# Performance work log

Measured on AMD Instinct MI355X. Metric: run time of the kernel, lower is better.

## Reference

```python
import jax, jax.numpy as jnp
import numpy as np

K_HOPS = 2  # SGConv K = nlayers


def setup_inputs() -> dict:
    key = jax.random.key(0)
    k1, k2, k3 = jax.random.split(key, 3)
    N, E, F, C = 100000, 1600000, 128, 40
    x = jax.random.normal(k1, (N, F), dtype=jnp.float32)
    edge_index = jax.random.randint(k2, (2, E), 0, N, dtype=jnp.int64)
    W = jax.random.normal(k3, (C, F), dtype=jnp.float32) * (1.0 / np.sqrt(F))
    b = jnp.zeros((C,), dtype=jnp.float32)
    return {"x": x, "edge_index": edge_index, "W": W, "b": b}


def reference(x, edge_index, W, b):
    # SGConv: K hops of GCN-normalized propagation (with self-loops), then Linear.
    N = x.shape[0]
    loop = jnp.arange(N, dtype=edge_index.dtype)
    src = jnp.concatenate([edge_index[0], loop])  # message source
    dst = jnp.concatenate([edge_index[1], loop])  # aggregation target
    w = jnp.ones(src.shape[0], dtype=x.dtype)     # edge_weight=None -> 1, self-loop fill=1
    deg = jax.ops.segment_sum(w, dst, num_segments=N)  # in-degree incl. self-loop (>=1)
    dinv = jax.lax.rsqrt(deg)
    norm = dinv[src] * w * dinv[dst]              # D^{-1/2} A D^{-1/2}
    h = x
    for _ in range(K_HOPS):
        h = jax.ops.segment_sum(norm[:, None] * h[src], dst, num_segments=N)
    return h @ W.T + b
```

## Files before the change

### kernel.cpp

```cpp
#include <hip/hip_runtime.h>
#include <hip/hip_fp16.h>
#include <cstdint>

#define CDIM 40
#define FDIM 128
#define BIN_SHIFT 8
#define BIN_SZ (1 << BIN_SHIFT)
#define CHUNK 4096
#define STAGE_CAP 8192

typedef _Float16 f16x8 __attribute__((ext_vector_type(8)));
typedef float f32x4 __attribute__((ext_vector_type(4)));

static __device__ __forceinline__ long long load_idx(const void* p, int is64, long long i) {
    if (is64) return ((const long long*)p)[i];
    return (long long)((const int*)p)[i];
}

static __device__ __forceinline__ unsigned packh2(float a, float b) {
    __half2 h;
    h.x = __float2half(a);
    h.y = __float2half(b);
    return *(unsigned*)&h;
}

static __device__ __forceinline__ void addv2(float* acc, uint2 v) {
    const __half2* h = (const __half2*)&v;
    float2 f0 = __half22float2(h[0]);
    float2 f1 = __half22float2(h[1]);
    acc[0] += f0.x; acc[1] += f0.y; acc[2] += f1.x; acc[3] += f1.y;
}

static __device__ __forceinline__ f16x8 cvt8(float4 a, float4 b) {
    f16x8 r;
    r[0] = (_Float16)a.x; r[1] = (_Float16)a.y; r[2] = (_Float16)a.z; r[3] = (_Float16)a.w;
    r[4] = (_Float16)b.x; r[5] = (_Float16)b.y; r[6] = (_Float16)b.z; r[7] = (_Float16)b.w;
    return r;
}

__global__ void k_init(int* cursor, int nb, int capRec) {
    int i = blockIdx.x * blockDim.x + threadIdx.x;
    if (i < nb) cursor[i] = i * capRec;
}

__global__ __launch_bounds__(256) void kA3(const void* ei, long long E,
                                           int nb, int* __restrict__ cursor,
                                           unsigned* __restrict__ binned) {
    __shared__ unsigned lval[CHUNK];
    __shared__ unsigned short lbin[CHUNK];
    __shared__ int lcnt[512];
    __shared__ int lbase[512];
    __shared__ int lflag;
    int tid = threadIdx.x;
    if (tid == 0) lflag = 1;
    for (int i = tid; i < nb; i += 256) lcnt[i] = 0;
    __syncthreads();
    {
        const unsigned* w = (const unsigned*)ei;
        int nscan = (int)((2 * E < 4096) ? (2 * E) : 4096);
        for (int k = 1 + 2 * tid; k < nscan; k += 512)
            if (w[k] != 0u) lflag = 0;
    }
    __syncthreads();
    int is64 = lflag;
    long long base = (long long)blockIdx.x * CHUNK;
    int nk = (int)min((long long)CHUNK, E - base);
    for (int k = tid; k < nk; k += 256) {
        long long e = base + k;
        int s = (int)load_idx(ei, is64, e);
        int d = (int)load_idx(ei, is64, E + e);
        int bin = d >> BIN_SHIFT;
        lval[k] = (unsigned)s | ((unsigned)(d & (BIN_SZ - 1)) << 17);
        lbin[k] = (unsigned short)bin;
        atomicAdd(&lcnt[bin], 1);
    }
    __syncthreads();
    for (int i = tid; i < nb; i += 256) {
        int c = lcnt[i];
        lbase[i] = c ? atomicAdd(&cursor[i], c) : 0;
        lcnt[i] = 0;
    }
    __syncthreads();
    for (int k = tid; k < nk; k += 256) {
        int bin = lbin[k];
        int loc = atomicAdd(&lcnt[bin], 1);
        binned[lbase[bin] + loc] = lval[k];
    }
}

__global__ __launch_bounds__(256) void kB(const unsigned* __restrict__ binned,
                                          const int* __restrict__ cursor,
                                          int capRec, int capC,
                                          int2* __restrict__ meta,
                                          float* __restrict__ dinv,
                                          int* __restrict__ cursorG,
                                          int* __restrict__ csr, int N) {
    __shared__ int lcnt[BIN_SZ];
    __shared__ int lexcl[BIN_SZ];
    __shared__ int ls[256];
    __shared__ int dh[64];
    __shared__ int tot;
    __shared__ int stage[STAGE_CAP];
    int b = blockIdx.x, tid = threadIdx.x;
    int node0 = b << BIN_SHIFT;
    int nn = min(BIN_SZ, N - node0);
    int recBase = b * capRec;
    int csrBase = b * capC;
    int nedges = cursor[b] - recBase;

    lcnt[tid] = 0;
    if (tid < 64) dh[tid] = 0;
    __syncthreads();
    for (int t = tid; t < nedges; t += 256)
        atomicAdd(&lcnt[(binned[recBase + t] >> 17) & (BIN_SZ - 1)], 1);
    __syncthreads();
    int myc = lcnt[tid];
    int psz = (myc + 3) & ~3;
    ls[tid] = psz;
    __syncthreads();
    for (int off = 1; off < 256; off <<= 1) {
        int t = (tid >= off) ? ls[tid - off] : 0;
        __syncthreads();
        ls[tid] += t;
        __syncthreads();
    }
    int ex = ls[tid] - psz;
    lexcl[tid] = ex;
    if (tid == 255) tot = ls[255];
    if (tid < nn) {
        dinv[node0 + tid] = rsqrtf(1.0f + (float)myc);
        atomicAdd(&dh[min(myc, 63)], 1);
    }
    __syncthreads();
    int total = tot;
    int dv = (tid < 64) ? dh[tid] : 0;
    ls[tid] = dv;
    __syncthreads();
    for (int off = 1; off < 64; off <<= 1) {
        int t = (tid >= off) ? ls[tid - off] : 0;
        __syncthreads();
        ls[tid] += t;
        __syncthreads();
    }
    if (tid < 64) dh[tid] = ls[tid] - dv;
    __syncthreads();
    if (tid < nn) {
        int pos = atomicAdd(&dh[min(myc, 63)], 1);
        int2 mi;
        mi.x = csrBase + ex;
        mi.y = (node0 + tid) | (myc << 17);
        meta[node0 + pos] = mi;
    }
    __syncthreads();
    lcnt[tid] = ex;
    __syncthreads();
    if (total <= STAGE_CAP) {
        for (int t = tid; t < total; t += 256) stage[t] = N;
        __syncthreads();
        for (int t = tid; t < nedges; t += 256) {
            unsigned v = binned[recBase + t];
            int src = (int)(v & 0x1FFFFu);
            int dl  = (int)((v >> 17) & (BIN_SZ - 1));
            int p = atomicAdd(&lcnt[dl], 1);
            stage[p] = src;
        }
        __syncthreads();
        const int4* sp = (const int4*)stage;
        int4* cp = (int4*)(csr + csrBase);
        for (int t = tid; t < (total >> 2); t += 256) cp[t] = sp[t];
    } else {
        if (tid < nn) cursorG[node0 + tid] = csrBase + ex;
        __syncthreads();
        for (int t = tid; t < nedges; t += 256) {
            unsigned v = binned[recBase + t];
            int src = (int)(v & 0x1FFFFu);
            int dl  = (int)((v >> 17) & (BIN_SZ - 1));
            int p = atomicAdd(&cursorG[node0 + dl], 1);
            csr[p] = src;
        }
        if (tid < nn)
            for (int k = myc; k < psz; ++k) csr[csrBase + ex + k] = N;
    }
}

__global__ __launch_bounds__(256) void k_gemm(const float* __restrict__ x,
                                              const float* __restrict__ W,
                                              const float* __restrict__ dinv,
                                              __half* __restrict__ gA,
                                              __half* __restrict__ gB, int N) {
    if (blockIdx.x == 0 && threadIdx.x < 20) {
        if (threadIdx.x < 16) ((unsigned*)(gA + (size_t)N * 32))[threadIdx.x] = 0u;
        else                  ((unsigned*)(gB + (size_t)N * 8))[threadIdx.x - 16] = 0u;
    }
    int wave = threadIdx.x >> 6;
    int lane = threadIdx.x & 63;
    int m = lane & 15;
    int quad = lane >> 4;
    f16x8 bfrag[3][4];
#pragma unroll
    for (int t = 0; t < 3; ++t) {
        int c = t * 16 + m;
#pragma unroll
        for (int q = 0; q < 4; ++q) {
            if (c < CDIM) {
                const float* wp = W + (size_t)c * FDIM + q * 32 + quad * 8;
                float4 w0 = *(const float4*)wp;
                float4 w1 = *(const float4*)(wp + 4);
                bfrag[t][q] = cvt8(w0, w1);
            } else {
                f16x8 z = {0, 0, 0, 0, 0, 0, 0, 0};
                bfrag[t][q] = z;
            }
        }
    }
#pragma unroll
    for (int i = 0; i < 4; ++i) {
        int nodebase = blockIdx.x * 256 + wave * 64 + i * 16;
        if (nodebase >= N) break;
        const float* xp = x + (size_t)(nodebase + m) * FDIM + quad * 8;
        f16x8 afrag[4];
#pragma unroll
        for (int q = 0; q < 4; ++q) {
            float4 x0 = *(const float4*)(xp + q * 32);
            float4 x1 = *(const float4*)(xp + q * 32 + 4);
            afrag[q] = cvt8(x0, x1);
        }
        f32x4 acc0 = {0, 0, 0, 0}, acc1 = {0, 0, 0, 0}, acc2 = {0, 0, 0, 0};
#pragma unroll
        for (int q = 0; q < 4; ++q) {
            acc0 = __builtin_amdgcn_mfma_f32_16x16x32_f16(afrag[q], bfrag[0][q], acc0, 0, 0, 0);
            acc1 = __builtin_amdgcn_mfma_f32_16x16x32_f16(afrag[q], bfrag[1][q], acc1, 0, 0, 0);
            acc2 = __builtin_amdgcn_mfma_f32_16x16x32_f16(afrag[q], bfrag[2][q], acc2, 0, 0, 0);
        }
        float4 dvv = *(const float4*)&dinv[nodebase + quad * 4];
        float ds[4] = {dvv.x, dvv.y, dvv.z, dvv.w};
#pragma unroll
        for (int r = 0; r < 4; ++r) {
            int node = nodebase + quad * 4 + r;
            gA[(size_t)node * 32 + m]      = __float2half(acc0[r] * ds[r]);
            gA[(size_t)node * 32 + 16 + m] = __float2half(acc1[r] * ds[r]);
            if (m < 8)
                gB[(size_t)node * 8 + m]   = __float2half(acc2[r] * ds[r]);
        }
    }
}

__global__ __launch_bounds__(256) void k_gather(const int2* __restrict__ meta,
                                                const int* __restrict__ csr,
                                                const __half* __restrict__ gA,
                                                const __half* __restrict__ gB,
                                                const float* __restrict__ b,
                                                __half* __restrict__ goA,
                                                __half* __restrict__ goB,
                                                float* __restrict__ outF,
                                                int N, int mode) {
    unsigned t = blockIdx.x * 256 + threadIdx.x;
    if (mode == 0 && t < 20) {
        if (t < 16) ((unsigned*)(goA + (size_t)N * 32))[t] = 0u;
        else        ((unsigned*)(goB + (size_t)N * 8))[t - 16] = 0u;
    }
    unsigned gidx = t / 10, c = t - gidx * 10;
    if (gidx >= (unsigned)N) return;
    int2 mi = meta[gidx];
    int j = mi.x;
    int node = mi.y & 0x1FFFF;
    int deg = mi.y >> 17;
    int end_pad = j + ((deg + 3) & ~3);
    const uint2* src;
    unsigned stride;
    if (c < 8) { src = (const uint2*)gA + c;       stride = 8; }
    else       { src = (const uint2*)gB + (c - 8); stride = 2; }
    float acc[4] = {0.0f, 0.0f, 0.0f, 0.0f};
    addv2(acc, src[(size_t)node * stride]);
    for (; j + 8 <= end_pad; j += 8) {
        int4 c0 = *(const int4*)&csr[j];
        int4 c1 = *(const int4*)&csr[j + 4];
        uint2 v0 = src[(size_t)c0.x * stride];
        uint2 v1 = src[(size_t)c0.y * stride];
        uint2 v2 = src[(size_t)c0.z * stride];
        uint2 v3 = src[(size_t)c0.w * stride];
        uint2 v4 = src[(size_t)c1.x * stride];
        uint2 v5 = src[(size_t)c1.y * stride];
        uint2 v6 = src[(size_t)c1.z * stride];
        uint2 v7 = src[(size_t)c1.w * stride];
        addv2(acc, v0); addv2(acc, v1); addv2(acc, v2); addv2(acc, v3);
        addv2(acc, v4); addv2(acc, v5); addv2(acc, v6); addv2(acc, v7);
    }
    if (j < end_pad) {
        int4 c0 = *(const int4*)&csr[j];
        uint2 v0 = src[(size_t)c0.x * stride];
        uint2 v1 = src[(size_t)c0.y * stride];
        uint2 v2 = src[(size_t)c0.z * stride];
        uint2 v3 = src[(size_t)c0.w * stride];
        addv2(acc, v0); addv2(acc, v1); addv2(acc, v2); addv2(acc, v3);
    }
    float d = rsqrtf(1.0f + (float)deg);
    if (mode == 0) {
        float s = d * d;
        uint2 o;
        o.x = packh2(acc[0] * s, acc[1] * s);
        o.y = packh2(acc[2] * s, acc[3] * s);
        if (c < 8) ((uint2*)goA)[(size_t)node * 8 + c] = o;
        else       ((uint2*)goB)[(size_t)node * 2 + (c - 8)] = o;
    } else {
        float4 bv = ((const float4*)b)[c];
        float4 o;
        o.x = acc[0] * d + bv.x;
        o.y = acc[1] * d + bv.y;
        o.z = acc[2] * d + bv.z;
        o.w = acc[3] * d + bv.w;
        ((float4*)outF)[(size_t)node * 10 + c] = o;
    }
}

static inline size_t align256(size_t v) { return (v + 255) & ~(size_t)255; }

extern "C" void kernel_launch(void* const* d_in, const int* in_sizes, int n_in,
                              void* d_out, int out_size, void* d_ws, size_t ws_size,
                              hipStream_t stream) {
    const float* x  = (const float*)d_in[0];
    const void*  ei = d_in[1];
    const float* W  = (const float*)d_in[2];
    const float* b  = (const float*)d_in[3];
    float* out = (float*)d_out;

    const int N = in_sizes[0] / FDIM;
    const long long E = (long long)in_sizes[1] / 2;

    const int nb     = (N + BIN_SZ - 1) >> BIN_SHIFT;
    const int nchunk = (int)((E + CHUNK - 1) / CHUNK);
    int capRec = (int)(E / nb) + 2048;
    if (capRec > STAGE_CAP) capRec = STAGE_CAP;
    int capC = (capRec + BIN_SZ * 3 + 1027) & ~3;

    char* wsb = (char*)d_ws;
    size_t off = 0;
    int*      cursor  = (int*)(wsb + off);      off = align256(off + (size_t)nb * 4);
    int*      cursorG = (int*)(wsb + off);      off = align256(off + (size_t)N * 4);
    int2*     meta    = (int2*)(wsb + off);     off = align256(off + (size_t)N * 8);
    float*    dinv    = (float*)(wsb + off);    off = align256(off + (size_t)N * 4);
    __half*   gA0     = (__half*)(wsb + off);   off = align256(off + (size_t)(N + 1) * 32 * 2);
    __half*   gB0     = (__half*)(wsb + off);   off = align256(off + (size_t)(N + 1) * 8 * 2);
    __half*   gA1     = (__half*)(wsb + off);   off = align256(off + (size_t)(N + 1) * 32 * 2);
    __half*   gB1     = (__half*)(wsb + off);   off = align256(off + (size_t)(N + 1) * 8 * 2);
    unsigned* binned  = (unsigned*)(wsb + off); off = align256(off + (size_t)nb * capRec * 4);
    int*      csr     = (int*)(wsb + off);      off = align256(off + (size_t)nb * capC * 4);

    const int B = 256;
    const int nbGE = (N + 255) / 256;
    const unsigned GT = 10u * (unsigned)N;
    const int nbGA = (int)((GT + B - 1) / B);

    k_init  <<<(nb + 255) / 256, 256, 0, stream>>>(cursor, nb, capRec);
    kA3     <<<nchunk, B, 0, stream>>>(ei, E, nb, cursor, binned);
    kB      <<<nb, B, 0, stream>>>(binned, cursor, capRec, capC, meta, dinv, cursorG, csr, N);
    k_gemm  <<<nbGE, B, 0, stream>>>(x, W, dinv, gA0, gB0, N);
    k_gather<<<nbGA, B, 0, stream>>>(meta, csr, gA0, gB0, b, gA1, gB1, nullptr, N, 0);
    k_gather<<<nbGA, B, 0, stream>>>(meta, csr, gA1, gB1, b, nullptr, nullptr, out, N, 1);
}
```

Measured before the change: 214.5 us.

## Split 40-channel propagated features into two 20-channel halves gathered separately

The projected fp16 features are now stored as two separate 20-channel arrays (40 bytes per node each) instead of a 32+8 split. Each hop runs two gather passes, one per half, so each pass's random-access working set is half the size and more likely to stay in L2/MALL. csr index loads and output stores become nontemporal to avoid polluting cache. The cost is reading the CSR index array twice per hop, doubled kernel launches, and 40-byte rows that are not aligned to 64-byte lines.

```diff
diff --git a/kernel.cpp b/kernel.cpp
--- a/kernel.cpp
+++ b/kernel.cpp
@@ -11,6 +11,8 @@
 
 typedef _Float16 f16x8 __attribute__((ext_vector_type(8)));
 typedef float f32x4 __attribute__((ext_vector_type(4)));
+typedef int i32x4 __attribute__((ext_vector_type(4)));
+typedef unsigned u32x2 __attribute__((ext_vector_type(2)));
 
 static __device__ __forceinline__ long long load_idx(const void* p, int is64, long long i) {
     if (is64) return ((const long long*)p)[i];
@@ -186,11 +188,11 @@
 __global__ __launch_bounds__(256) void k_gemm(const float* __restrict__ x,
                                               const float* __restrict__ W,
                                               const float* __restrict__ dinv,
-                                              __half* __restrict__ gA,
-                                              __half* __restrict__ gB, int N) {
+                                              __half* __restrict__ gL,
+                                              __half* __restrict__ gH, int N) {
     if (blockIdx.x == 0 && threadIdx.x < 20) {
-        if (threadIdx.x < 16) ((unsigned*)(gA + (size_t)N * 32))[threadIdx.x] = 0u;
-        else                  ((unsigned*)(gB + (size_t)N * 8))[threadIdx.x - 16] = 0u;
+        if (threadIdx.x < 10) ((unsigned*)(gL + (size_t)N * 20))[threadIdx.x] = 0u;
+        else                  ((unsigned*)(gH + (size_t)N * 20))[threadIdx.x - 10] = 0u;
     }
     int wave = threadIdx.x >> 6;
     int lane = threadIdx.x & 63;
@@ -237,79 +239,74 @@
 #pragma unroll
         for (int r = 0; r < 4; ++r) {
             int node = nodebase + quad * 4 + r;
-            gA[(size_t)node * 32 + m]      = __float2half(acc0[r] * ds[r]);
-            gA[(size_t)node * 32 + 16 + m] = __float2half(acc1[r] * ds[r]);
+            float v0 = acc0[r] * ds[r];
+            float v1 = acc1[r] * ds[r];
+            gL[(size_t)node * 20 + m] = __float2half(v0);
+            if (m < 4) gL[(size_t)node * 20 + 16 + m] = __float2half(v1);
+            else       gH[(size_t)node * 20 + (m - 4)] = __float2half(v1);
             if (m < 8)
-                gB[(size_t)node * 8 + m]   = __float2half(acc2[r] * ds[r]);
+                gH[(size_t)node * 20 + 12 + m] = __float2half(acc2[r] * ds[r]);
         }
     }
 }
 
 __global__ __launch_bounds__(256) void k_gather(const int2* __restrict__ meta,
                                                 const int* __restrict__ csr,
-                                                const __half* __restrict__ gA,
-                                                const __half* __restrict__ gB,
+                                                const __half* __restrict__ gin,
                                                 const float* __restrict__ b,
-                                                __half* __restrict__ goA,
-                                                __half* __restrict__ goB,
+                                                __half* __restrict__ gout,
                                                 float* __restrict__ outF,
-                                                int N, int mode) {
+                                                int N, int mode, int pass) {
     unsigned t = blockIdx.x * 256 + threadIdx.x;
-    if (mode == 0 && t < 20) {
-        if (t < 16) ((unsigned*)(goA + (size_t)N * 32))[t] = 0u;
-        else        ((unsigned*)(goB + (size_t)N * 8))[t - 16] = 0u;
-    }
-    unsigned gidx = t / 10, c = t - gidx * 10;
+    if (mode == 0 && t < 10)
+        ((unsigned*)(gout + (size_t)N * 20))[t] = 0u;
+    unsigned gidx = t / 5, c = t - gidx * 5;
     if (gidx >= (unsigned)N) return;
     int2 mi = meta[gidx];
     int j = mi.x;
     int node = mi.y & 0x1FFFF;
     int deg = mi.y >> 17;
     int end_pad = j + ((deg + 3) & ~3);
-    const uint2* src;
-    unsigned stride;
-    if (c < 8) { src = (const uint2*)gA + c;       stride = 8; }
-    else       { src = (const uint2*)gB + (c - 8); stride = 2; }
+    const uint2* src = (const uint2*)gin + c;
     float acc[4] = {0.0f, 0.0f, 0.0f, 0.0f};
-    addv2(acc, src[(size_t)node * stride]);
+    addv2(acc, src[(size_t)node * 5]);
     for (; j + 8 <= end_pad; j += 8) {
-        int4 c0 = *(const int4*)&csr[j];
-        int4 c1 = *(const int4*)&csr[j + 4];
-        uint2 v0 = src[(size_t)c0.x * stride];
-        uint2 v1 = src[(size_t)c0.y * stride];
-        uint2 v2 = src[(size_t)c0.z * stride];
-        uint2 v3 = src[(size_t)c0.w * stride];
-        uint2 v4 = src[(size_t)c1.x * stride];
-        uint2 v5 = src[(size_t)c1.y * stride];
-        uint2 v6 = src[(size_t)c1.z * stride];
-        uint2 v7 = src[(size_t)c1.w * stride];
+        i32x4 c0 = __builtin_nontemporal_load((const i32x4*)&csr[j]);
+        i32x4 c1 = __builtin_nontemporal_load((const i32x4*)&csr[j + 4]);
+        uint2 v0 = src[(size_t)c0.x * 5];
+        uint2 v1 = src[(size_t)c0.y * 5];
+        uint2 v2 = src[(size_t)c0.z * 5];
+        uint2 v3 = src[(size_t)c0.w * 5];
+        uint2 v4 = src[(size_t)c1.x * 5];
+        uint2 v5 = src[(size_t)c1.y * 5];
+        uint2 v6 = src[(size_t)c1.z * 5];
+        uint2 v7 = src[(size_t)c1.w * 5];
         addv2(acc, v0); addv2(acc, v1); addv2(acc, v2); addv2(acc, v3);
         addv2(acc, v4); addv2(acc, v5); addv2(acc, v6); addv2(acc, v7);
     }
     if (j < end_pad) {
-        int4 c0 = *(const int4*)&csr[j];
-        uint2 v0 = src[(size_t)c0.x * stride];
-        uint2 v1 = src[(size_t)c0.y * stride];
-        uint2 v2 = src[(size_t)c0.z * stride];
-        uint2 v3 = src[(size_t)c0.w * stride];
+        i32x4 c0 = __builtin_nontemporal_load((const i32x4*)&csr[j]);
+        uint2 v0 = src[(size_t)c0.x * 5];
+        uint2 v1 = src[(size_t)c0.y * 5];
+        uint2 v2 = src[(size_t)c0.z * 5];
+        uint2 v3 = src[(size_t)c0.w * 5];
         addv2(acc, v0); addv2(acc, v1); addv2(acc, v2); addv2(acc, v3);
     }
     float d = rsqrtf(1.0f + (float)deg);
     if (mode == 0) {
         float s = d * d;
-        uint2 o;
+        u32x2 o;
         o.x = packh2(acc[0] * s, acc[1] * s);
         o.y = packh2(acc[2] * s, acc[3] * s);
-        if (c < 8) ((uint2*)goA)[(size_t)node * 8 + c] = o;
-        else       ((uint2*)goB)[(size_t)node * 2 + (c - 8)] = o;
+        __builtin_nontemporal_store(o, (u32x2*)gout + (size_t)node * 5 + c);
     } else {
-        float4 bv = ((const float4*)b)[c];
-        float4 o;
-        o.x = acc[0] * d + bv.x;
-        o.y = acc[1] * d + bv.y;
-        o.z = acc[2] * d + bv.z;
-        o.w = acc[3] * d + bv.w;
-        ((float4*)outF)[(size_t)node * 10 + c] = o;
+        float4 bv = ((const float4*)(b + pass * 20))[c];
+        f32x4 o;
+        o[0] = acc[0] * d + bv.x;
+        o[1] = acc[1] * d + bv.y;
+        o[2] = acc[2] * d + bv.z;
+        o[3] = acc[3] * d + bv.w;
+        __builtin_nontemporal_store(o, (f32x4*)outF + (size_t)node * 10 + pass * 5 + c);
     }
 }
 
@@ -339,22 +336,24 @@
     int*      cursorG = (int*)(wsb + off);      off = align256(off + (size_t)N * 4);
     int2*     meta    = (int2*)(wsb + off);     off = align256(off + (size_t)N * 8);
     float*    dinv    = (float*)(wsb + off);    off = align256(off + (size_t)N * 4);
-    __half*   gA0     = (__half*)(wsb + off);   off = align256(off + (size_t)(N + 1) * 32 * 2);
-    __half*   gB0     = (__half*)(wsb + off);   off = align256(off + (size_t)(N + 1) * 8 * 2);
-    __half*   gA1     = (__half*)(wsb + off);   off = align256(off + (size_t)(N + 1) * 32 * 2);
-    __half*   gB1     = (__half*)(wsb + off);   off = align256(off + (size_t)(N + 1) * 8 * 2);
+    __half*   g0L     = (__half*)(wsb + off);   off = align256(off + (size_t)(N + 1) * 20 * 2);
+    __half*   g0H     = (__half*)(wsb + off);   off = align256(off + (size_t)(N + 1) * 20 * 2);
+    __half*   g1L     = (__half*)(wsb + off);   off = align256(off + (size_t)(N + 1) * 20 * 2);
+    __half*   g1H     = (__half*)(wsb + off);   off = align256(off + (size_t)(N + 1) * 20 * 2);
     unsigned* binned  = (unsigned*)(wsb + off); off = align256(off + (size_t)nb * capRec * 4);
     int*      csr     = (int*)(wsb + off);      off = align256(off + (size_t)nb * capC * 4);
 
     const int B = 256;
     const int nbGE = (N + 255) / 256;
-    const unsigned GT = 10u * (unsigned)N;
+    const unsigned GT = 5u * (unsigned)N;
     const int nbGA = (int)((GT + B - 1) / B);
 
     k_init  <<<(nb + 255) / 256, 256, 0, stream>>>(cursor, nb, capRec);
     kA3     <<<nchunk, B, 0, stream>>>(ei, E, nb, cursor, binned);
     kB      <<<nb, B, 0, stream>>>(binned, cursor, capRec, capC, meta, dinv, cursorG, csr, N);
-    k_gemm  <<<nbGE, B, 0, stream>>>(x, W, dinv, gA0, gB0, N);
-    k_gather<<<nbGA, B, 0, stream>>>(meta, csr, gA0, gB0, b, gA1, gB1, nullptr, N, 0);
-    k_gather<<<nbGA, B, 0, stream>>>(meta, csr, gA1, gB1, b, nullptr, nullptr, out, N, 1);
-}
+    k_gemm  <<<nbGE, B, 0, stream>>>(x, W, dinv, g0L, g0H, N);
+    k_gather<<<nbGA, B, 0, stream>>>(meta, csr, g0L, b, g1L, nullptr, N, 0, 0);
+    k_gather<<<nbGA, B, 0, stream>>>(meta, csr, g0H, b, g1H, nullptr, N, 0, 1);
+    k_gather<<<nbGA, B, 0, stream>>>(meta, csr, g1L, b, nullptr, out, N, 1, 0);
+    k_gather<<<nbGA, B, 0, stream>>>(meta, csr, g1H, b, nullptr, out, N, 1, 1);
+}
```

After: 252.9 us. 17.9% more time.

## Fuse all stages into one persistent cooperative kernel with grid syncs

Applied to the files above, without the earlier changes.

Replaces the six separate launches (init, binning, CSR build, GEMM, two gather hops) with a single persistent cooperative kernel that loops over work and separates phases with grid.sync. The GEMM is also folded into the CSR-build loop per bin, using a shared-memory dinv, so the dinv global round trip is dropped. The aim is to cut launch gaps and inter-kernel tails. In exchange, occupancy is limited by the larger shared-memory union, and grid-wide barriers plus fewer resident blocks may reduce latency hiding in the gather phases. The old multi-kernel path stays as a fallback.

```diff
diff --git a/kernel.cpp b/kernel.cpp
--- a/kernel.cpp
+++ b/kernel.cpp
@@ -1,4 +1,5 @@
 #include <hip/hip_runtime.h>
+#include <hip/hip_cooperative_groups.h>
 #include <hip/hip_fp16.h>
 #include <cstdint>
 
@@ -12,6 +13,8 @@
 typedef _Float16 f16x8 __attribute__((ext_vector_type(8)));
 typedef float f32x4 __attribute__((ext_vector_type(4)));
 
+namespace cg = cooperative_groups;
+
 static __device__ __forceinline__ long long load_idx(const void* p, int is64, long long i) {
     if (is64) return ((const long long*)p)[i];
     return (long long)((const int*)p)[i];
@@ -38,229 +41,51 @@
     return r;
 }
 
-__global__ void k_init(int* cursor, int nb, int capRec) {
-    int i = blockIdx.x * blockDim.x + threadIdx.x;
-    if (i < nb) cursor[i] = i * capRec;
-}
-
-__global__ __launch_bounds__(256) void kA3(const void* ei, long long E,
-                                           int nb, int* __restrict__ cursor,
-                                           unsigned* __restrict__ binned) {
-    __shared__ unsigned lval[CHUNK];
-    __shared__ unsigned short lbin[CHUNK];
-    __shared__ int lcnt[512];
-    __shared__ int lbase[512];
-    __shared__ int lflag;
-    int tid = threadIdx.x;
-    if (tid == 0) lflag = 1;
-    for (int i = tid; i < nb; i += 256) lcnt[i] = 0;
-    __syncthreads();
-    {
-        const unsigned* w = (const unsigned*)ei;
-        int nscan = (int)((2 * E < 4096) ? (2 * E) : 4096);
-        for (int k = 1 + 2 * tid; k < nscan; k += 512)
-            if (w[k] != 0u) lflag = 0;
-    }
-    __syncthreads();
-    int is64 = lflag;
-    long long base = (long long)blockIdx.x * CHUNK;
-    int nk = (int)min((long long)CHUNK, E - base);
-    for (int k = tid; k < nk; k += 256) {
-        long long e = base + k;
-        int s = (int)load_idx(ei, is64, e);
-        int d = (int)load_idx(ei, is64, E + e);
-        int bin = d >> BIN_SHIFT;
-        lval[k] = (unsigned)s | ((unsigned)(d & (BIN_SZ - 1)) << 17);
-        lbin[k] = (unsigned short)bin;
-        atomicAdd(&lcnt[bin], 1);
-    }
-    __syncthreads();
-    for (int i = tid; i < nb; i += 256) {
-        int c = lcnt[i];
-        lbase[i] = c ? atomicAdd(&cursor[i], c) : 0;
-        lcnt[i] = 0;
-    }
-    __syncthreads();
-    for (int k = tid; k < nk; k += 256) {
-        int bin = lbin[k];
-        int loc = atomicAdd(&lcnt[bin], 1);
-        binned[lbase[bin] + loc] = lval[k];
-    }
-}
-
-__global__ __launch_bounds__(256) void kB(const unsigned* __restrict__ binned,
-                                          const int* __restrict__ cursor,
-                                          int capRec, int capC,
-                                          int2* __restrict__ meta,
-                                          float* __restrict__ dinv,
-                                          int* __restrict__ cursorG,
-                                          int* __restrict__ csr, int N) {
-    __shared__ int lcnt[BIN_SZ];
-    __shared__ int lexcl[BIN_SZ];
-    __shared__ int ls[256];
-    __shared__ int dh[64];
-    __shared__ int tot;
-    __shared__ int stage[STAGE_CAP];
-    int b = blockIdx.x, tid = threadIdx.x;
-    int node0 = b << BIN_SHIFT;
-    int nn = min(BIN_SZ, N - node0);
-    int recBase = b * capRec;
-    int csrBase = b * capC;
-    int nedges = cursor[b] - recBase;
-
-    lcnt[tid] = 0;
-    if (tid < 64) dh[tid] = 0;
-    __syncthreads();
-    for (int t = tid; t < nedges; t += 256)
-        atomicAdd(&lcnt[(binned[recBase + t] >> 17) & (BIN_SZ - 1)], 1);
-    __syncthreads();
-    int myc = lcnt[tid];
-    int psz = (myc + 3) & ~3;
-    ls[tid] = psz;
-    __syncthreads();
-    for (int off = 1; off < 256; off <<= 1) {
-        int t = (tid >= off) ? ls[tid - off] : 0;
-        __syncthreads();
-        ls[tid] += t;
-        __syncthreads();
-    }
-    int ex = ls[tid] - psz;
-    lexcl[tid] = ex;
-    if (tid == 255) tot = ls[255];
-    if (tid < nn) {
-        dinv[node0 + tid] = rsqrtf(1.0f + (float)myc);
-        atomicAdd(&dh[min(myc, 63)], 1);
-    }
-    __syncthreads();
-    int total = tot;
-    int dv = (tid < 64) ? dh[tid] : 0;
-    ls[tid] = dv;
-    __syncthreads();
-    for (int off = 1; off < 64; off <<= 1) {
-        int t = (tid >= off) ? ls[tid - off] : 0;
-        __syncthreads();
-        ls[tid] += t;
-        __syncthreads();
-    }
-    if (tid < 64) dh[tid] = ls[tid] - dv;
-    __syncthreads();
-    if (tid < nn) {
-        int pos = atomicAdd(&dh[min(myc, 63)], 1);
-        int2 mi;
-        mi.x = csrBase + ex;
-        mi.y = (node0 + tid) | (myc << 17);
-        meta[node0 + pos] = mi;
-    }
-    __syncthreads();
-    lcnt[tid] = ex;
-    __syncthreads();
-    if (total <= STAGE_CAP) {
-        for (int t = tid; t < total; t += 256) stage[t] = N;
-        __syncthreads();
-        for (int t = tid; t < nedges; t += 256) {
-            unsigned v = binned[recBase + t];
-            int src = (int)(v & 0x1FFFFu);
-            int dl  = (int)((v >> 17) & (BIN_SZ - 1));
-            int p = atomicAdd(&lcnt[dl], 1);
-            stage[p] = src;
-        }
-        __syncthreads();
-        const int4* sp = (const int4*)stage;
-        int4* cp = (int4*)(csr + csrBase);
-        for (int t = tid; t < (total >> 2); t += 256) cp[t] = sp[t];
-    } else {
-        if (tid < nn) cursorG[node0 + tid] = csrBase + ex;
-        __syncthreads();
-        for (int t = tid; t < nedges; t += 256) {
-            unsigned v = binned[recBase + t];
-            int src = (int)(v & 0x1FFFFu);
-            int dl  = (int)((v >> 17) & (BIN_SZ - 1));
-            int p = atomicAdd(&cursorG[node0 + dl], 1);
-            csr[p] = src;
-        }
-        if (tid < nn)
-            for (int k = myc; k < psz; ++k) csr[csrBase + ex + k] = N;
-    }
-}
-
-__global__ __launch_bounds__(256) void k_gemm(const float* __restrict__ x,
-                                              const float* __restrict__ W,
-                                              const float* __restrict__ dinv,
-                                              __half* __restrict__ gA,
-                                              __half* __restrict__ gB, int N) {
-    if (blockIdx.x == 0 && threadIdx.x < 20) {
-        if (threadIdx.x < 16) ((unsigned*)(gA + (size_t)N * 32))[threadIdx.x] = 0u;
-        else                  ((unsigned*)(gB + (size_t)N * 8))[threadIdx.x - 16] = 0u;
-    }
-    int wave = threadIdx.x >> 6;
-    int lane = threadIdx.x & 63;
-    int m = lane & 15;
-    int quad = lane >> 4;
-    f16x8 bfrag[3][4];
-#pragma unroll
-    for (int t = 0; t < 3; ++t) {
-        int c = t * 16 + m;
-#pragma unroll
-        for (int q = 0; q < 4; ++q) {
-            if (c < CDIM) {
-                const float* wp = W + (size_t)c * FDIM + q * 32 + quad * 8;
-                float4 w0 = *(const float4*)wp;
-                float4 w1 = *(const float4*)(wp + 4);
-                bfrag[t][q] = cvt8(w0, w1);
-            } else {
-                f16x8 z = {0, 0, 0, 0, 0, 0, 0, 0};
-                bfrag[t][q] = z;
-            }
-        }
-    }
-#pragma unroll
-    for (int i = 0; i < 4; ++i) {
-        int nodebase = blockIdx.x * 256 + wave * 64 + i * 16;
-        if (nodebase >= N) break;
-        const float* xp = x + (size_t)(nodebase + m) * FDIM + quad * 8;
-        f16x8 afrag[4];
-#pragma unroll
-        for (int q = 0; q < 4; ++q) {
-            float4 x0 = *(const float4*)(xp + q * 32);
-            float4 x1 = *(const float4*)(xp + q * 32 + 4);
-            afrag[q] = cvt8(x0, x1);
-        }
-        f32x4 acc0 = {0, 0, 0, 0}, acc1 = {0, 0, 0, 0}, acc2 = {0, 0, 0, 0};
-#pragma unroll
-        for (int q = 0; q < 4; ++q) {
-            acc0 = __builtin_amdgcn_mfma_f32_16x16x32_f16(afrag[q], bfrag[0][q], acc0, 0, 0, 0);
-            acc1 = __builtin_amdgcn_mfma_f32_16x16x32_f16(afrag[q], bfrag[1][q], acc1, 0, 0, 0);
-            acc2 = __builtin_amdgcn_mfma_f32_16x16x32_f16(afrag[q], bfrag[2][q], acc2, 0, 0, 0);
-        }
-        float4 dvv = *(const float4*)&dinv[nodebase + quad * 4];
-        float ds[4] = {dvv.x, dvv.y, dvv.z, dvv.w};
-#pragma unroll
-        for (int r = 0; r < 4; ++r) {
-            int node = nodebase + quad * 4 + r;
-            gA[(size_t)node * 32 + m]      = __float2half(acc0[r] * ds[r]);
-            gA[(size_t)node * 32 + 16 + m] = __float2half(acc1[r] * ds[r]);
-            if (m < 8)
-                gB[(size_t)node * 8 + m]   = __float2half(acc2[r] * ds[r]);
-        }
-    }
-}
-
-__global__ __launch_bounds__(256) void k_gather(const int2* __restrict__ meta,
-                                                const int* __restrict__ csr,
-                                                const __half* __restrict__ gA,
-                                                const __half* __restrict__ gB,
-                                                const float* __restrict__ b,
-                                                __half* __restrict__ goA,
-                                                __half* __restrict__ goB,
-                                                float* __restrict__ outF,
-                                                int N, int mode) {
-    unsigned t = blockIdx.x * 256 + threadIdx.x;
-    if (mode == 0 && t < 20) {
-        if (t < 16) ((unsigned*)(goA + (size_t)N * 32))[t] = 0u;
-        else        ((unsigned*)(goB + (size_t)N * 8))[t - 16] = 0u;
-    }
+
+struct SMemA {
+    unsigned lval[CHUNK];
+    unsigned short lbin[CHUNK];
+    int lcnt[512];
+    int lbase[512];
+    int flag;
+};
+struct SMemB {
+    int lcnt[BIN_SZ];
+    int lexcl[BIN_SZ];
+    int ls[256];
+    int dh[64];
+    int tot;
+    float dinvL[BIN_SZ];
+    int stage[STAGE_CAP];
+};
+union SMem {
+    SMemA a;
+    SMemB b;
+};
+
+struct FusedArgs {
+    const float* x;
+    const void* ei;
+    const float* W;
+    const float* bias;
+    float* out;
+    int* cursor;
+    int2* meta;
+    int* cursorG;
+    __half* gA0; __half* gB0; __half* gA1; __half* gB1;
+    unsigned* binned;
+    int* csr;
+    long long E;
+    int N, nb, nchunk, capRec, capC;
+};
+
+static __device__ __forceinline__ void gather_one(
+    const int2* __restrict__ meta, const int* __restrict__ csr,
+    const __half* __restrict__ gA, const __half* __restrict__ gB,
+    const float* __restrict__ bias,
+    __half* __restrict__ goA, __half* __restrict__ goB,
+    float* __restrict__ outF, int N, int mode, unsigned t) {
     unsigned gidx = t / 10, c = t - gidx * 10;
-    if (gidx >= (unsigned)N) return;
     int2 mi = meta[gidx];
     int j = mi.x;
     int node = mi.y & 0x1FFFF;
@@ -303,7 +128,7 @@
         if (c < 8) ((uint2*)goA)[(size_t)node * 8 + c] = o;
         else       ((uint2*)goB)[(size_t)node * 2 + (c - 8)] = o;
     } else {
-        float4 bv = ((const float4*)b)[c];
+        float4 bv = ((const float4*)bias)[c];
         float4 o;
         o.x = acc[0] * d + bv.x;
         o.y = acc[1] * d + bv.y;
@@ -311,6 +136,438 @@
         o.w = acc[3] * d + bv.w;
         ((float4*)outF)[(size_t)node * 10 + c] = o;
     }
+}
+
+__global__ __launch_bounds__(256) void k_fused(FusedArgs P) {
+    __shared__ SMem sm;
+    cg::grid_group grid = cg::this_grid();
+    const int tid = threadIdx.x;
+    const unsigned gtid = blockIdx.x * 256 + tid;
+    const unsigned gsz = gridDim.x * 256;
+
+    for (unsigned i = gtid; i < (unsigned)P.nb; i += gsz)
+        P.cursor[i] = (int)i * P.capRec;
+    if (gtid < 40) {
+        if (gtid < 16)      ((unsigned*)(P.gA0 + (size_t)P.N * 32))[gtid] = 0u;
+        else if (gtid < 20) ((unsigned*)(P.gB0 + (size_t)P.N * 8))[gtid - 16] = 0u;
+        else if (gtid < 36) ((unsigned*)(P.gA1 + (size_t)P.N * 32))[gtid - 20] = 0u;
+        else                ((unsigned*)(P.gB1 + (size_t)P.N * 8))[gtid - 36] = 0u;
+    }
+    grid.sync();
+
+    {
+        if (tid == 0) sm.a.flag = 1;
+        __syncthreads();
+        {
+            const unsigned* w = (const unsigned*)P.ei;
+            int nscan = (int)((2 * P.E < 4096) ? (2 * P.E) : 4096);
+            for (int k = 1 + 2 * tid; k < nscan; k += 512)
+                if (w[k] != 0u) sm.a.flag = 0;
+        }
+        __syncthreads();
+        int is64 = sm.a.flag;
+        for (int chunk = blockIdx.x; chunk < P.nchunk; chunk += gridDim.x) {
+            for (int i = tid; i < P.nb; i += 256) sm.a.lcnt[i] = 0;
+            __syncthreads();
+            long long base = (long long)chunk * CHUNK;
+            int nk = (int)min((long long)CHUNK, P.E - base);
+            for (int k = tid; k < nk; k += 256) {
+                long long e = base + k;
+                int s = (int)load_idx(P.ei, is64, e);
+                int d = (int)load_idx(P.ei, is64, P.E + e);
+                int bin = d >> BIN_SHIFT;
+                sm.a.lval[k] = (unsigned)s | ((unsigned)(d & (BIN_SZ - 1)) << 17);
+                sm.a.lbin[k] = (unsigned short)bin;
+                atomicAdd(&sm.a.lcnt[bin], 1);
+            }
+            __syncthreads();
+            for (int i = tid; i < P.nb; i += 256) {
+                int c = sm.a.lcnt[i];
+                sm.a.lbase[i] = c ? atomicAdd(&P.cursor[i], c) : 0;
+                sm.a.lcnt[i] = 0;
+            }
+            __syncthreads();
+            for (int k = tid; k < nk; k += 256) {
+                int bin = sm.a.lbin[k];
+                int loc = atomicAdd(&sm.a.lcnt[bin], 1);
+                P.binned[sm.a.lbase[bin] + loc] = sm.a.lval[k];
+            }
+            __syncthreads();
+        }
+    }
+    grid.sync();
+
+    const int wave = tid >> 6;
+    const int lane = tid & 63;
+    const int m = lane & 15;
+    const int quad = lane >> 4;
+    f16x8 bfrag[3][4];
+#pragma unroll
+    for (int t = 0; t < 3; ++t) {
+        int c = t * 16 + m;
+#pragma unroll
+        for (int q = 0; q < 4; ++q) {
+            if (c < CDIM) {
+                const float* wp = P.W + (size_t)c * FDIM + q * 32 + quad * 8;
+                float4 w0 = *(const float4*)wp;
+                float4 w1 = *(const float4*)(wp + 4);
+                bfrag[t][q] = cvt8(w0, w1);
+            } else {
+                f16x8 z = {0, 0, 0, 0, 0, 0, 0, 0};
+                bfrag[t][q] = z;
+            }
+        }
+    }
+    for (int b = blockIdx.x; b < P.nb; b += gridDim.x) {
+        int node0 = b << BIN_SHIFT;
+        int nn = min(BIN_SZ, P.N - node0);
+        int recBase = b * P.capRec;
+        int csrBase = b * P.capC;
+        int nedges = P.cursor[b] - recBase;
+
+        sm.b.lcnt[tid] = 0;
+        if (tid < 64) sm.b.dh[tid] = 0;
+        __syncthreads();
+        for (int t = tid; t < nedges; t += 256)
+            atomicAdd(&sm.b.lcnt[(P.binned[recBase + t] >> 17) & (BIN_SZ - 1)], 1);
+        __syncthreads();
+        int myc = sm.b.lcnt[tid];
+        int psz = (myc + 3) & ~3;
+        sm.b.ls[tid] = psz;
+        __syncthreads();
+        for (int off = 1; off < 256; off <<= 1) {
+            int t = (tid >= off) ? sm.b.ls[tid - off] : 0;
+            __syncthreads();
+            sm.b.ls[tid] += t;
+            __syncthreads();
+        }
+        int ex = sm.b.ls[tid] - psz;
+        sm.b.lexcl[tid] = ex;
+        if (tid == 255) sm.b.tot = sm.b.ls[255];
+        if (tid < nn) {
+            sm.b.dinvL[tid] = rsqrtf(1.0f + (float)myc);
+            atomicAdd(&sm.b.dh[min(myc, 63)], 1);
+        }
+        __syncthreads();
+        int total = sm.b.tot;
+        int dv = (tid < 64) ? sm.b.dh[tid] : 0;
+        sm.b.ls[tid] = dv;
+        __syncthreads();
+        for (int off = 1; off < 64; off <<= 1) {
+            int t = (tid >= off) ? sm.b.ls[tid - off] : 0;
+            __syncthreads();
+            sm.b.ls[tid] += t;
+            __syncthreads();
+        }
+        if (tid < 64) sm.b.dh[tid] = sm.b.ls[tid] - dv;
+        __syncthreads();
+        if (tid < nn) {
+            int pos = atomicAdd(&sm.b.dh[min(myc, 63)], 1);
+            int2 mi;
+            mi.x = csrBase + ex;
+            mi.y = (node0 + tid) | (myc << 17);
+            P.meta[node0 + pos] = mi;
+        }
+        __syncthreads();
+        sm.b.lcnt[tid] = ex;
+        __syncthreads();
+        if (total <= STAGE_CAP) {
+            for (int t = tid; t < total; t += 256) sm.b.stage[t] = P.N;
+            __syncthreads();
+            for (int t = tid; t < nedges; t += 256) {
+                unsigned v = P.binned[recBase + t];
+                int src = (int)(v & 0x1FFFFu);
+                int dl  = (int)((v >> 17) & (BIN_SZ - 1));
+                int p = atomicAdd(&sm.b.lcnt[dl], 1);
+                sm.b.stage[p] = src;
+            }
+            __syncthreads();
+            const int4* sp = (const int4*)sm.b.stage;
+            int4* cp = (int4*)(P.csr + csrBase);
+            for (int t = tid; t < (total >> 2); t += 256) cp[t] = sp[t];
+        } else {
+            if (tid < nn) P.cursorG[node0 + tid] = csrBase + ex;
+            __syncthreads();
+            for (int t = tid; t < nedges; t += 256) {
+                unsigned v = P.binned[recBase + t];
+                int src = (int)(v & 0x1FFFFu);
+                int dl  = (int)((v >> 17) & (BIN_SZ - 1));
+                int p = atomicAdd(&P.cursorG[node0 + dl], 1);
+                P.csr[p] = src;
+            }
+            if (tid < nn)
+                for (int k = myc; k < psz; ++k) P.csr[csrBase + ex + k] = P.N;
+        }
+        __syncthreads();
+#pragma unroll
+        for (int i = 0; i < 4; ++i) {
+            int lnode = wave * 64 + i * 16;
+            int nodebase = node0 + lnode;
+            if (nodebase >= P.N) break;
+            const float* xp = P.x + (size_t)(nodebase + m) * FDIM + quad * 8;
+            f16x8 afrag[4];
+#pragma unroll
+            for (int q = 0; q < 4; ++q) {
+                float4 x0 = *(const float4*)(xp + q * 32);
+                float4 x1 = *(const float4*)(xp + q * 32 + 4);
+                afrag[q] = cvt8(x0, x1);
+            }
+            f32x4 acc0 = {0, 0, 0, 0}, acc1 = {0, 0, 0, 0}, acc2 = {0, 0, 0, 0};
+#pragma unroll
+            for (int q = 0; q < 4; ++q) {
+                acc0 = __builtin_amdgcn_mfma_f32_16x16x32_f16(afrag[q], bfrag[0][q], acc0, 0, 0, 0);
+                acc1 = __builtin_amdgcn_mfma_f32_16x16x32_f16(afrag[q], bfrag[1][q], acc1, 0, 0, 0);
+                acc2 = __builtin_amdgcn_mfma_f32_16x16x32_f16(afrag[q], bfrag[2][q], acc2, 0, 0, 0);
+            }
+            float ds[4];
+#pragma unroll
+            for (int r = 0; r < 4; ++r) ds[r] = sm.b.dinvL[lnode + quad * 4 + r];
+#pragma unroll
+            for (int r = 0; r < 4; ++r) {
+                int node = nodebase + quad * 4 + r;
+                P.gA0[(size_t)node * 32 + m]      = __float2half(acc0[r] * ds[r]);
+                P.gA0[(size_t)node * 32 + 16 + m] = __float2half(acc1[r] * ds[r]);
+                if (m < 8)
+                    P.gB0[(size_t)node * 8 + m]   = __float2half(acc2[r] * ds[r]);
+            }
+        }
+        __syncthreads();
+    }
+    grid.sync();
+
+    unsigned GT = 10u * (unsigned)P.N;
+    for (unsigned t = gtid; t < GT; t += gsz)
+        gather_one(P.meta, P.csr, P.gA0, P.gB0, P.bias, P.gA1, P.gB1, nullptr, P.N, 0, t);
+    grid.sync();
+
+    for (unsigned t = gtid; t < GT; t += gsz)
+        gather_one(P.meta, P.csr, P.gA1, P.gB1, P.bias, nullptr, nullptr, P.out, P.N, 1, t);
+}
+
+
+__global__ void k_init(int* cursor, int nb, int capRec) {
+    int i = blockIdx.x * blockDim.x + threadIdx.x;
+    if (i < nb) cursor[i] = i * capRec;
+}
+
+__global__ __launch_bounds__(256) void kA3(const void* ei, long long E,
+                                           int nb, int* __restrict__ cursor,
+                                           unsigned* __restrict__ binned) {
+    __shared__ unsigned lval[CHUNK];
+    __shared__ unsigned short lbin[CHUNK];
+    __shared__ int lcnt[512];
+    __shared__ int lbase[512];
+    __shared__ int lflag;
+    int tid = threadIdx.x;
+    if (tid == 0) lflag = 1;
+    for (int i = tid; i < nb; i += 256) lcnt[i] = 0;
+    __syncthreads();
+    {
+        const unsigned* w = (const unsigned*)ei;
+        int nscan = (int)((2 * E < 4096) ? (2 * E) : 4096);
+        for (int k = 1 + 2 * tid; k < nscan; k += 512)
+            if (w[k] != 0u) lflag = 0;
+    }
+    __syncthreads();
+    int is64 = lflag;
+    long long base = (long long)blockIdx.x * CHUNK;
+    int nk = (int)min((long long)CHUNK, E - base);
+    for (int k = tid; k < nk; k += 256) {
+        long long e = base + k;
+        int s = (int)load_idx(ei, is64, e);
+        int d = (int)load_idx(ei, is64, E + e);
+        int bin = d >> BIN_SHIFT;
+        lval[k] = (unsigned)s | ((unsigned)(d & (BIN_SZ - 1)) << 17);
+        lbin[k] = (unsigned short)bin;
+        atomicAdd(&lcnt[bin], 1);
+    }
+    __syncthreads();
+    for (int i = tid; i < nb; i += 256) {
+        int c = lcnt[i];
+        lbase[i] = c ? atomicAdd(&cursor[i], c) : 0;
+        lcnt[i] = 0;
+    }
+    __syncthreads();
+    for (int k = tid; k < nk; k += 256) {
+        int bin = lbin[k];
+        int loc = atomicAdd(&lcnt[bin], 1);
+        binned[lbase[bin] + loc] = lval[k];
+    }
+}
+
+__global__ __launch_bounds__(256) void kB(const unsigned* __restrict__ binned,
+                                          const int* __restrict__ cursor,
+                                          int capRec, int capC,
+                                          int2* __restrict__ meta,
+                                          float* __restrict__ dinv,
+                                          int* __restrict__ cursorG,
+                                          int* __restrict__ csr, int N) {
+    __shared__ int lcnt[BIN_SZ];
+    __shared__ int lexcl[BIN_SZ];
+    __shared__ int ls[256];
+    __shared__ int dh[64];
+    __shared__ int tot;
+    __shared__ int stage[STAGE_CAP];
+    int b = blockIdx.x, tid = threadIdx.x;
+    int node0 = b << BIN_SHIFT;
+    int nn = min(BIN_SZ, N - node0);
+    int recBase = b * capRec;
+    int csrBase = b * capC;
+    int nedges = cursor[b] - recBase;
+
+    lcnt[tid] = 0;
+    if (tid < 64) dh[tid] = 0;
+    __syncthreads();
+    for (int t = tid; t < nedges; t += 256)
+        atomicAdd(&lcnt[(binned[recBase + t] >> 17) & (BIN_SZ - 1)], 1);
+    __syncthreads();
+    int myc = lcnt[tid];
+    int psz = (myc + 3) & ~3;
+    ls[tid] = psz;
+    __syncthreads();
+    for (int off = 1; off < 256; off <<= 1) {
+        int t = (tid >= off) ? ls[tid - off] : 0;
+        __syncthreads();
+        ls[tid] += t;
+        __syncthreads();
+    }
+    int ex = ls[tid] - psz;
+    lexcl[tid] = ex;
+    if (tid == 255) tot = ls[255];
+    if (tid < nn) {
+        dinv[node0 + tid] = rsqrtf(1.0f + (float)myc);
+        atomicAdd(&dh[min(myc, 63)], 1);
+    }
+    __syncthreads();
+    int total = tot;
+    int dv = (tid < 64) ? dh[tid] : 0;
+    ls[tid] = dv;
+    __syncthreads();
+    for (int off = 1; off < 64; off <<= 1) {
+        int t = (tid >= off) ? ls[tid - off] : 0;
+        __syncthreads();
+        ls[tid] += t;
+        __syncthreads();
+    }
+    if (tid < 64) dh[tid] = ls[tid] - dv;
+    __syncthreads();
+    if (tid < nn) {
+        int pos = atomicAdd(&dh[min(myc, 63)], 1);
+        int2 mi;
+        mi.x = csrBase + ex;
+        mi.y = (node0 + tid) | (myc << 17);
+        meta[node0 + pos] = mi;
+    }
+    __syncthreads();
+    lcnt[tid] = ex;
+    __syncthreads();
+    if (total <= STAGE_CAP) {
+        for (int t = tid; t < total; t += 256) stage[t] = N;
+        __syncthreads();
+        for (int t = tid; t < nedges; t += 256) {
+            unsigned v = binned[recBase + t];
+            int src = (int)(v & 0x1FFFFu);
+            int dl  = (int)((v >> 17) & (BIN_SZ - 1));
+            int p = atomicAdd(&lcnt[dl], 1);
+            stage[p] = src;
+        }
+        __syncthreads();
+        const int4* sp = (const int4*)stage;
+        int4* cp = (int4*)(csr + csrBase);
+        for (int t = tid; t < (total >> 2); t += 256) cp[t] = sp[t];
+    } else {
+        if (tid < nn) cursorG[node0 + tid] = csrBase + ex;
+        __syncthreads();
+        for (int t = tid; t < nedges; t += 256) {
+            unsigned v = binned[recBase + t];
+            int src = (int)(v & 0x1FFFFu);
+            int dl  = (int)((v >> 17) & (BIN_SZ - 1));
+            int p = atomicAdd(&cursorG[node0 + dl], 1);
+            csr[p] = src;
+        }
+        if (tid < nn)
+            for (int k = myc; k < psz; ++k) csr[csrBase + ex + k] = N;
+    }
+}
+
+__global__ __launch_bounds__(256) void k_gemm(const float* __restrict__ x,
+                                              const float* __restrict__ W,
+                                              const float* __restrict__ dinv,
+                                              __half* __restrict__ gA,
+                                              __half* __restrict__ gB, int N) {
+    if (blockIdx.x == 0 && threadIdx.x < 20) {
+        if (threadIdx.x < 16) ((unsigned*)(gA + (size_t)N * 32))[threadIdx.x] = 0u;
+        else                  ((unsigned*)(gB + (size_t)N * 8))[threadIdx.x - 16] = 0u;
+    }
+    int wave = threadIdx.x >> 6;
+    int lane = threadIdx.x & 63;
+    int m = lane & 15;
+    int quad = lane >> 4;
+    f16x8 bfrag[3][4];
+#pragma unroll
+    for (int t = 0; t < 3; ++t) {
+        int c = t * 16 + m;
+#pragma unroll
+        for (int q = 0; q < 4; ++q) {
+            if (c < CDIM) {
+                const float* wp = W + (size_t)c * FDIM + q * 32 + quad * 8;
+                float4 w0 = *(const float4*)wp;
+                float4 w1 = *(const float4*)(wp + 4);
+                bfrag[t][q] = cvt8(w0, w1);
+            } else {
+                f16x8 z = {0, 0, 0, 0, 0, 0, 0, 0};
+                bfrag[t][q] = z;
+            }
+        }
+    }
+#pragma unroll
+    for (int i = 0; i < 4; ++i) {
+        int nodebase = blockIdx.x * 256 + wave * 64 + i * 16;
+        if (nodebase >= N) break;
+        const float* xp = x + (size_t)(nodebase + m) * FDIM + quad * 8;
+        f16x8 afrag[4];
+#pragma unroll
+        for (int q = 0; q < 4; ++q) {
+            float4 x0 = *(const float4*)(xp + q * 32);
+            float4 x1 = *(const float4*)(xp + q * 32 + 4);
+            afrag[q] = cvt8(x0, x1);
+        }
+        f32x4 acc0 = {0, 0, 0, 0}, acc1 = {0, 0, 0, 0}, acc2 = {0, 0, 0, 0};
+#pragma unroll
+        for (int q = 0; q < 4; ++q) {
+            acc0 = __builtin_amdgcn_mfma_f32_16x16x32_f16(afrag[q], bfrag[0][q], acc0, 0, 0, 0);
+            acc1 = __builtin_amdgcn_mfma_f32_16x16x32_f16(afrag[q], bfrag[1][q], acc1, 0, 0, 0);
+            acc2 = __builtin_amdgcn_mfma_f32_16x16x32_f16(afrag[q], bfrag[2][q], acc2, 0, 0, 0);
+        }
+        float4 dvv = *(const float4*)&dinv[nodebase + quad * 4];
+        float ds[4] = {dvv.x, dvv.y, dvv.z, dvv.w};
+#pragma unroll
+        for (int r = 0; r < 4; ++r) {
+            int node = nodebase + quad * 4 + r;
+            gA[(size_t)node * 32 + m]      = __float2half(acc0[r] * ds[r]);
+            gA[(size_t)node * 32 + 16 + m] = __float2half(acc1[r] * ds[r]);
+            if (m < 8)
+                gB[(size_t)node * 8 + m]   = __float2half(acc2[r] * ds[r]);
+        }
+    }
+}
+
+__global__ __launch_bounds__(256) void k_gather(const int2* __restrict__ meta,
+                                                const int* __restrict__ csr,
+                                                const __half* __restrict__ gA,
+                                                const __half* __restrict__ gB,
+                                                const float* __restrict__ b,
+                                                __half* __restrict__ goA,
+                                                __half* __restrict__ goB,
+                                                float* __restrict__ outF,
+                                                int N, int mode) {
+    unsigned t = blockIdx.x * 256 + threadIdx.x;
+    if (mode == 0 && t < 20) {
+        if (t < 16) ((unsigned*)(goA + (size_t)N * 32))[t] = 0u;
+        else        ((unsigned*)(goB + (size_t)N * 8))[t - 16] = 0u;
+    }
+    if (t >= 10u * (unsigned)N) return;
+    gather_one(meta, csr, gA, gB, b, goA, goB, outF, N, mode, t);
 }
 
 static inline size_t align256(size_t v) { return (v + 255) & ~(size_t)255; }
@@ -346,15 +603,44 @@
     unsigned* binned  = (unsigned*)(wsb + off); off = align256(off + (size_t)nb * capRec * 4);
     int*      csr     = (int*)(wsb + off);      off = align256(off + (size_t)nb * capC * 4);
 
-    const int B = 256;
-    const int nbGE = (N + 255) / 256;
-    const unsigned GT = 10u * (unsigned)N;
-    const int nbGA = (int)((GT + B - 1) / B);
-
-    k_init  <<<(nb + 255) / 256, 256, 0, stream>>>(cursor, nb, capRec);
-    kA3     <<<nchunk, B, 0, stream>>>(ei, E, nb, cursor, binned);
-    kB      <<<nb, B, 0, stream>>>(binned, cursor, capRec, capC, meta, dinv, cursorG, csr, N);
-    k_gemm  <<<nbGE, B, 0, stream>>>(x, W, dinv, gA0, gB0, N);
-    k_gather<<<nbGA, B, 0, stream>>>(meta, csr, gA0, gB0, b, gA1, gB1, nullptr, N, 0);
-    k_gather<<<nbGA, B, 0, stream>>>(meta, csr, gA1, gB1, b, nullptr, nullptr, out, N, 1);
-}
+    static int occ = -2;
+    static int nCU = 0;
+    if (occ == -2) {
+        int v = 0;
+        hipError_t e = hipOccupancyMaxActiveBlocksPerMultiprocessor(&v, k_fused, 256, 0);
+        occ = (e == hipSuccess && v > 0) ? v : 0;
+        hipDeviceProp_t prop;
+        nCU = (hipGetDeviceProperties(&prop, 0) == hipSuccess) ? prop.multiProcessorCount : 256;
+    }
+
+    bool launched = false;
+    if (occ > 0) {
+        FusedArgs A;
+        A.x = x; A.ei = ei; A.W = W; A.bias = b; A.out = out;
+        A.cursor = cursor; A.meta = meta; A.cursorG = cursorG;
+        A.gA0 = gA0; A.gB0 = gB0; A.gA1 = gA1; A.gB1 = gB1;
+        A.binned = binned; A.csr = csr;
+        A.E = E; A.N = N; A.nb = nb; A.nchunk = nchunk; A.capRec = capRec; A.capC = capC;
+        void* args[] = { (void*)&A };
+        int G = occ * nCU;
+        int maxNeed = (int)((10u * (unsigned)N + 255) / 256);
+        if (G > maxNeed) G = maxNeed;
+        if (G < 1) G = 1;
+        hipError_t e = hipLaunchCooperativeKernel((const void*)k_fused, dim3(G), dim3(256),
+                                                  args, 0, stream);
+        launched = (e == hipSuccess);
+    }
+
+    if (!launched) {
+        const int B = 256;
+        const int nbGE = (N + 255) / 256;
+        const unsigned GT = 10u * (unsigned)N;
+        const int nbGA = (int)((GT + B - 1) / B);
+        k_init  <<<(nb + 255) / 256, 256, 0, stream>>>(cursor, nb, capRec);
+        kA3     <<<nchunk, B, 0, stream>>>(ei, E, nb, cursor, binned);
+        kB      <<<nb, B, 0, stream>>>(binned, cursor, capRec, capC, meta, dinv, cursorG, csr, N);
+        k_gemm  <<<nbGE, B, 0, stream>>>(x, W, dinv, gA0, gB0, N);
+        k_gather<<<nbGA, B, 0, stream>>>(meta, csr, gA0, gB0, b, gA1, gB1, nullptr, N, 0);
+        k_gather<<<nbGA, B, 0, stream>>>(meta, csr, gA1, gB1, b, nullptr, nullptr, out, N, 1);
+    }
+}
```

New measurement: 470.9 us. +119.5%, slower.
